# Kernel tuning notes

Measured on AMD Instinct MI355X. Metric: run time of the kernel, lower is better.

Reference implementation:

```python
import jax, jax.numpy as jnp
import numpy as np

BS, N1, N2, D = 2, 512, 512, 64  # in_dim = out_dim = D
TEMP = 1.0
EPS = 1e-5
POOL_RATIO = 0.5


def setup_inputs() -> dict:
    key = jax.random.key(0)
    ks = iter(jax.random.split(key, 32))
    nrm = lambda shape, s=0.05: jax.random.normal(next(ks), shape, dtype=jnp.float32) * s
    inp = {
        "x1": jax.random.normal(next(ks), (BS, N1, D), dtype=jnp.float32),
        "x2": jax.random.normal(next(ks), (BS, N2, D), dtype=jnp.float32),
        # proj_type1 / proj_type2 (Linear in->in); weights stored [in, out]
        "W1": nrm((D, D)), "b1": jnp.zeros((D,), jnp.float32),
        "W2": nrm((D, D)), "b2": jnp.zeros((D,), jnp.float32),
        # att_proj / att_projM (Linear in->out)
        "Wa": nrm((D, D)), "ba": jnp.zeros((D,), jnp.float32),
        "WaM": nrm((D, D)), "baM": jnp.zeros((D,), jnp.float32),
        # attention weight vectors (out_dim, 1)
        "w11": nrm((D, 1), 0.2), "w22": nrm((D, 1), 0.2),
        "w12": nrm((D, 1), 0.2), "wM": nrm((D, 1), 0.2),
        # projections
        "Wpa": nrm((D, D)), "bpa": jnp.zeros((D,), jnp.float32),
        "Wwoa": nrm((D, D)), "bwoa": jnp.zeros((D,), jnp.float32),
        "WpaM": nrm((D, D)), "bpaM": jnp.zeros((D,), jnp.float32),
        "WwoaM": nrm((D, D)), "bwoaM": jnp.zeros((D,), jnp.float32),
        # BatchNorm1d affine params
        "gamma": jnp.ones((D,), jnp.float32), "beta": jnp.zeros((D,), jnp.float32),
        # GraphPool score layer (Linear D->1), shared pool as in Model
        "Wp": nrm((D, 1), 0.2), "bp": jnp.zeros((1,), jnp.float32),
    }
    return inp


def _htrg_gat(x1, x2, W1, b1, W2, b2, Wa, ba, WaM, baM, w11, w22, w12, wM,
              Wpa, bpa, Wwoa, bwoa, WpaM, bpaM, WwoaM, bwoaM, gamma, beta):
    n1 = x1.shape[1]
    x1p = x1 @ W1 + b1
    x2p = x2 @ W2 + b2
    x = jnp.concatenate([x1p, x2p], axis=1)          # (b, N, d)
    master = jnp.mean(x, axis=1, keepdims=True)       # (b, 1, d)

    # --- attention map: pairwise node products, blockwise score weights ---
    pair = x[:, :, None, :] * x[:, None, :, :]        # (b, N, N, d)
    t = jnp.tanh(pair @ Wa + ba)                      # (b, N, N, d)
    top = jnp.concatenate([t[:, :n1, :n1] @ w11, t[:, :n1, n1:] @ w12], axis=2)
    bot = jnp.concatenate([t[:, n1:, :n1] @ w12, t[:, n1:, n1:] @ w22], axis=2)
    board = jnp.concatenate([top, bot], axis=1) / TEMP  # (b, N, N, 1)
    att = jax.nn.softmax(board, axis=-2)

    # --- master update ---
    tm = jnp.tanh((x * master) @ WaM + baM)           # (b, N, d)
    am = jax.nn.softmax((tm @ wM) / TEMP, axis=-2)    # (b, N, 1)
    agg_m = jnp.einsum('bn,bnd->bd', am[..., 0], x)[:, None, :]  # (b, 1, d)
    master_new = (agg_m @ WpaM + bpaM) + (master @ WwoaM + bwoaM)

    # --- project nodes with attention ---
    agg = jnp.einsum('bij,bjd->bid', att[..., 0], x)  # (b, N, d)
    xo = (agg @ Wpa + bpa) + (x @ Wwoa + bwoa)

    # --- BatchNorm1d over flattened (b*N) rows, then SELU ---
    mu = jnp.mean(xo, axis=(0, 1))
    var = jnp.var(xo, axis=(0, 1))
    xo = (xo - mu) * jax.lax.rsqrt(var + EPS) * gamma + beta
    xo = jax.nn.selu(xo)
    return xo[:, :n1], xo[:, n1:], master_new


def _graph_pool(x, Wp, bp):
    # scores -> sigmoid -> scale features -> top-k gather
    n = x.shape[1]
    k = max(int(n * POOL_RATIO), 1)
    scores = jax.nn.sigmoid(x @ Wp + bp)              # (b, n, 1)
    _, idx = jax.lax.top_k(scores[..., 0], k)         # (b, k)
    xs = x * scores
    return jnp.take_along_axis(xs, idx[..., None], axis=1)  # (b, k, d)


def reference(x1, x2, W1, b1, W2, b2, Wa, ba, WaM, baM, w11, w22, w12, wM,
              Wpa, bpa, Wwoa, bwoa, WpaM, bpaM, WwoaM, bwoaM, gamma, beta, Wp, bp):
    o1, o2, master = _htrg_gat(x1, x2, W1, b1, W2, b2, Wa, ba, WaM, baM,
                               w11, w22, w12, wM, Wpa, bpa, Wwoa, bwoa,
                               WpaM, bpaM, WwoaM, bwoaM, gamma, beta)
    p1 = _graph_pool(o1, Wp, bp)
    p2 = _graph_pool(o2, Wp, bp)
    return jnp.concatenate([p1, p2], axis=1)          # (b, n1/2 + n2/2, d)
```

## Files before the change

### kernel.cpp

```cpp
#include <hip/hip_runtime.h>

typedef float f32x4 __attribute__((ext_vector_type(4)));
typedef short short8 __attribute__((ext_vector_type(8)));
typedef short s16x4 __attribute__((ext_vector_type(4)));

#define N_TOT 1024
#define N_HALF 512
#define D 64
#define KPOOL 256

#if __has_builtin(__builtin_amdgcn_exp2f)
#define EXP2F(x) __builtin_amdgcn_exp2f(x)
#else
#define EXP2F(x) __expf((x) * 0.6931471805599453f)
#endif
#if __has_builtin(__builtin_amdgcn_rcpf)
#define RCPF(x) __builtin_amdgcn_rcpf(x)
#else
#define RCPF(x) (1.0f / (x))
#endif

__device__ __forceinline__ short f2bf(float v) {
    unsigned u = __float_as_uint(v);
    u += 0x7FFFu + ((u >> 16) & 1u);
    return (short)(u >> 16);
}
__device__ __forceinline__ float bf2f(unsigned short u) {
    return __uint_as_float(((unsigned)u) << 16);
}

__global__ void __launch_bounds__(64)
k_proj(const float* __restrict__ x1, const float* __restrict__ x2,
       const float* __restrict__ W1, const float* __restrict__ b1,
       const float* __restrict__ W2, const float* __restrict__ b2,
       float* __restrict__ x_f, unsigned short* __restrict__ x_bf,
       unsigned short* __restrict__ xT_hi, unsigned short* __restrict__ xT_lo) {
    int blk = blockIdx.x;
    int b = blk >> 8;
    int n0 = (blk & 255) * 4;
    int t = threadIdx.x;

    const float *src, *W, *bias;
    if (n0 < N_HALF) { src = x1 + (b * N_HALF + n0) * D;            W = W1; bias = b1; }
    else             { src = x2 + (b * N_HALF + (n0 - N_HALF)) * D; W = W2; bias = b2; }

    __shared__ float rows[4][D];
#pragma unroll
    for (int r = 0; r < 4; ++r) rows[r][t] = src[r * D + t];
    __syncthreads();

    float bv = bias[t];
    float acc[4];
#pragma unroll
    for (int r = 0; r < 4; ++r) acc[r] = bv;
    for (int d = 0; d < D; ++d) {
        float w = W[d * D + t];
#pragma unroll
        for (int r = 0; r < 4; ++r) acc[r] = fmaf(rows[r][d], w, acc[r]);
    }

    s16x4 hiv, lov;
#pragma unroll
    for (int r = 0; r < 4; ++r) {
        unsigned short hi = (unsigned short)f2bf(acc[r]);
        unsigned short lo = (unsigned short)f2bf(acc[r] - bf2f(hi));
        x_f[((size_t)b * N_TOT + n0 + r) * D + t] = acc[r];
        x_bf[((size_t)b * N_TOT + n0 + r) * D + t] = hi;
        hiv[r] = (short)hi; lov[r] = (short)lo;
    }
    *reinterpret_cast<s16x4*>(xT_hi + ((size_t)b * D + t) * N_TOT + n0) = hiv;
    *reinterpret_cast<s16x4*>(xT_lo + ((size_t)b * D + t) * N_TOT + n0) = lov;
}

__global__ void __launch_bounds__(256)
k_score(const float* __restrict__ x_f, const unsigned short* __restrict__ x_bf,
        const float* __restrict__ Wa, const float* __restrict__ ba,
        const float* __restrict__ w11, const float* __restrict__ w22,
        const float* __restrict__ w12, unsigned* __restrict__ Ep) {
    int bid = blockIdx.x;
    int b = bid >> 9, c = bid & 511;
    int tid = threadIdx.x;
    int l = tid & 63, wv = tid >> 6;
    int kc = l & 15, dg = l >> 4;

    const float C2 = 2.885390081777927f;
    const float LOG2E = 1.4426950408889634f;

    __shared__ float xi_s[D];
    const unsigned short* xb_b = x_bf + b * N_TOT * D;
    unsigned* Eb = Ep + ((size_t)b << 20);

#pragma unroll
    for (int phase = 0; phase < 2; ++phase) {
        int i = phase ? (N_TOT - 1 - c) : c;

        __syncthreads();
        if (tid < D) xi_s[tid] = x_f[(b * N_TOT + i) * D + tid];
        __syncthreads();

        const float* wTop = (i < N_HALF) ? w11 : w12;
        const float* wBot = (i < N_HALF) ? w12 : w22;

        short8 bfrag[4][2];
        float bac[4], wm2A[4], wm2B[4];
        float wsumA = 0.f, wsumB = 0.f;
#pragma unroll
        for (int kt = 0; kt < 4; ++kt) {
            int kcol = kt * 16 + kc;
            bac[kt] = ba[kcol] * C2;
            float wA = wTop[kcol], wB = wBot[kcol];
            wm2A[kt] = -2.f * wA; wm2B[kt] = -2.f * wB;
            wsumA += wA; wsumB += wB;
#pragma unroll
            for (int mm = 0; mm < 2; ++mm) {
                short8 f;
#pragma unroll
                for (int e = 0; e < 8; ++e) {
                    int d = mm * 32 + dg * 8 + e;
                    f[e] = f2bf(xi_s[d] * Wa[d * D + kcol]);
                }
                bfrag[kt][mm] = f;
            }
        }

        int jt0 = i >> 4;
        for (int jt = jt0 + wv; jt < 64; jt += 4) {
            const unsigned short* arow = xb_b + (jt * 16 + kc) * D + dg * 8;
            short8 a0 = *reinterpret_cast<const short8*>(arow);
            short8 a1 = *reinterpret_cast<const short8*>(arow + 32);
            f32x4 acc[4];
#pragma unroll
            for (int kt = 0; kt < 4; ++kt) {
                f32x4 z = {0.f, 0.f, 0.f, 0.f};
                z = __builtin_amdgcn_mfma_f32_16x16x32_bf16(a0, bfrag[kt][0], z, 0, 0, 0);
                z = __builtin_amdgcn_mfma_f32_16x16x32_bf16(a1, bfrag[kt][1], z, 0, 0, 0);
                acc[kt] = z;
            }
            bool top = (jt < 32);
            float wsum_t = top ? wsumA : wsumB;
#pragma unroll
            for (int r = 0; r < 4; ++r) {
                float part = wsum_t;
#pragma unroll
                for (int kt = 0; kt < 4; ++kt) {
                    float e2 = EXP2F(fmaf(acc[kt][r], C2, bac[kt]));
                    float rcv = RCPF(e2 + 1.f);
                    part = fmaf(top ? wm2A[kt] : wm2B[kt], rcv, part);
                }
                part += __shfl_xor(part, 1);
                part += __shfl_xor(part, 2);
                part += __shfl_xor(part, 4);
                part += __shfl_xor(part, 8);
                if (kc == 0) {
                    int j = jt * 16 + dg * 4 + r;
                    if (j >= i) {
                        float e = EXP2F(part * LOG2E);
                        unsigned short eh = (unsigned short)f2bf(e);
                        unsigned short el = (unsigned short)f2bf(e - bf2f(eh));
                        unsigned pk = ((unsigned)eh << 16) | (unsigned)el;
                        Eb[(size_t)i * N_TOT + j] = pk;
                        if (j > i) Eb[(size_t)j * N_TOT + i] = pk;
                    }
                }
            }
        }
    }
}

__global__ void __launch_bounds__(256)
k_aggp(const unsigned* __restrict__ Ep,
       const unsigned short* __restrict__ xT_hi, const unsigned short* __restrict__ xT_lo,
       float* __restrict__ pagg, float* __restrict__ rowsum_part) {
    int blk = blockIdx.x;
    int b = blk >> 7, rest = blk & 127;
    int it = rest >> 1, jh = rest & 1;
    int i0 = it * 16, jbase = jh * 512;
    int tid = threadIdx.x;
    int l = tid & 63, wv = tid >> 6;
    int kc = l & 15, dg = l >> 4;

    const unsigned* Eb = Ep + ((size_t)b << 20);
    const unsigned short* xTH = xT_hi + (size_t)b * D * N_TOT;
    const unsigned short* xTL = xT_lo + (size_t)b * D * N_TOT;

    f32x4 C0 = {0.f, 0.f, 0.f, 0.f}, C1 = C0, C2v = C0;
    const unsigned* Ap = Eb + (size_t)(i0 + kc) * N_TOT + jbase + dg * 8;
    const unsigned short* BH = xTH + (size_t)(wv * 16 + kc) * N_TOT + jbase + dg * 8;
    const unsigned short* BL = xTL + (size_t)(wv * 16 + kc) * N_TOT + jbase + dg * 8;
#pragma unroll 4
    for (int ks = 0; ks < 16; ++ks) {
        uint4 p0 = *reinterpret_cast<const uint4*>(Ap + ks * 32);
        uint4 p1 = *reinterpret_cast<const uint4*>(Ap + ks * 32 + 4);
        short8 ah, al;
        ah[0] = (short)(p0.x >> 16); al[0] = (short)(p0.x & 0xffff);
        ah[1] = (short)(p0.y >> 16); al[1] = (short)(p0.y & 0xffff);
        ah[2] = (short)(p0.z >> 16); al[2] = (short)(p0.z & 0xffff);
        ah[3] = (short)(p0.w >> 16); al[3] = (short)(p0.w & 0xffff);
        ah[4] = (short)(p1.x >> 16); al[4] = (short)(p1.x & 0xffff);
        ah[5] = (short)(p1.y >> 16); al[5] = (short)(p1.y & 0xffff);
        ah[6] = (short)(p1.z >> 16); al[6] = (short)(p1.z & 0xffff);
        ah[7] = (short)(p1.w >> 16); al[7] = (short)(p1.w & 0xffff);
        short8 bh = *reinterpret_cast<const short8*>(BH + ks * 32);
        short8 bl = *reinterpret_cast<const short8*>(BL + ks * 32);
        C0 = __builtin_amdgcn_mfma_f32_16x16x32_bf16(ah, bh, C0, 0, 0, 0);
        C1 = __builtin_amdgcn_mfma_f32_16x16x32_bf16(ah, bl, C1, 0, 0, 0);
        C2v = __builtin_amdgcn_mfma_f32_16x16x32_bf16(al, bh, C2v, 0, 0, 0);
    }
    f32x4 C = (C0 + C1) + C2v;

    {
        int row = wv * 4 + (l & 3);
        int seg = l >> 2;
        const unsigned* Er = Eb + (size_t)(i0 + row) * N_TOT + jbase + seg * 32;
        float rs = 0.f;
#pragma unroll
        for (int u = 0; u < 8; ++u) {
            uint4 v = *reinterpret_cast<const uint4*>(Er + u * 4);
            rs += __uint_as_float(v.x & 0xffff0000u) + __uint_as_float(v.x << 16);
            rs += __uint_as_float(v.y & 0xffff0000u) + __uint_as_float(v.y << 16);
            rs += __uint_as_float(v.z & 0xffff0000u) + __uint_as_float(v.z << 16);
            rs += __uint_as_float(v.w & 0xffff0000u) + __uint_as_float(v.w << 16);
        }
        rs += __shfl_xor(rs, 4);
        rs += __shfl_xor(rs, 8);
        rs += __shfl_xor(rs, 16);
        rs += __shfl_xor(rs, 32);
        if (l < 4) rowsum_part[(size_t)(b * 2 + jh) * N_TOT + i0 + wv * 4 + l] = rs;
    }

#pragma unroll
    for (int r = 0; r < 4; ++r)
        pagg[((size_t)(b * 2 + jh) * N_TOT + i0 + dg * 4 + r) * D + wv * 16 + kc] = C[r];
}

__global__ void __launch_bounds__(256)
k_aggfin(const float* __restrict__ pagg, const float* __restrict__ rowsum_part,
         const float* __restrict__ x_f,
         const float* __restrict__ Wpa, const float* __restrict__ bpa,
         const float* __restrict__ Wwoa, const float* __restrict__ bwoa,
         float* __restrict__ xo_pre, float* __restrict__ partials) {
    int b = blockIdx.x >> 6, it = blockIdx.x & 63;
    int i0 = it * 16;
    int tid = threadIdx.x;
    int l = tid & 63, wv = tid >> 6;

    __shared__ float aggL[16][D];
    __shared__ float xiL[16][D];
    __shared__ float xoL[16][D];
    __shared__ float riL[16];

    const float* p0 = pagg + ((size_t)(b * 2 + 0) * N_TOT + i0) * D;
    const float* p1 = pagg + ((size_t)(b * 2 + 1) * N_TOT + i0) * D;
    const float* xB = x_f + ((size_t)b * N_TOT + i0) * D;
#pragma unroll
    for (int u = 0; u < 4; ++u) {
        int idx = tid + u * 256;
        reinterpret_cast<float*>(aggL)[idx] = p0[idx] + p1[idx];
        reinterpret_cast<float*>(xiL)[idx] = xB[idx];
    }
    if (tid < 16)
        riL[tid] = 1.f / (rowsum_part[(size_t)(b * 2 + 0) * N_TOT + i0 + tid] +
                          rowsum_part[(size_t)(b * 2 + 1) * N_TOT + i0 + tid]);
    __syncthreads();
#pragma unroll
    for (int u = 0; u < 4; ++u) {
        int idx = tid + u * 256;
        reinterpret_cast<float*>(aggL)[idx] *= riL[idx >> 6];
    }
    __syncthreads();

    int k = l;
    float xo[4];
#pragma unroll
    for (int r = 0; r < 4; ++r) xo[r] = bpa[k] + bwoa[k];
    for (int dd = 0; dd < D; ++dd) {
        float wp = Wpa[dd * D + k], ww = Wwoa[dd * D + k];
#pragma unroll
        for (int r = 0; r < 4; ++r) {
            int row = wv * 4 + r;
            xo[r] += aggL[row][dd] * wp + xiL[row][dd] * ww;
        }
    }
#pragma unroll
    for (int r = 0; r < 4; ++r) {
        int row = wv * 4 + r;
        xo_pre[((size_t)b * N_TOT + i0 + row) * D + k] = xo[r];
        xoL[row][k] = xo[r];
    }
    __syncthreads();
    if (tid < D) {
        float s = 0.f, qv = 0.f;
#pragma unroll
        for (int mm = 0; mm < 16; ++mm) { float v = xoL[mm][tid]; s += v; qv = fmaf(v, v, qv); }
        partials[blockIdx.x * 128 + tid] = s;
        partials[blockIdx.x * 128 + 64 + tid] = qv;
    }
}

__global__ void k_stats2(const float* __restrict__ partials, float* __restrict__ stats) {
    int t = threadIdx.x;
    int g = t >> 7;
    int f128 = t & 127;
    float s = 0.f;
    for (int blk = g * 32; blk < g * 32 + 32; ++blk) s += partials[blk * 128 + f128];
    __shared__ float SQ[4][128];
    SQ[g][f128] = s;
    __syncthreads();
    if (t < 128) {
        float tot = SQ[0][t] + SQ[1][t] + SQ[2][t] + SQ[3][t];
        SQ[0][t] = tot;
    }
    __syncthreads();
    if (t < D) {
        float mu = SQ[0][t] * (1.f / 2048.f);
        float ex2 = SQ[0][64 + t] * (1.f / 2048.f);
        stats[t] = mu;
        stats[D + t] = rsqrtf(ex2 - mu * mu + 1e-5f);
    }
}

__global__ void k_norm(const float* __restrict__ xo_pre, const float* __restrict__ stats,
                       const float* __restrict__ gamma, const float* __restrict__ beta,
                       const float* __restrict__ Wp, const float* __restrict__ bp,
                       float* __restrict__ o_norm, float* __restrict__ scores) {
    int r = blockIdx.x * 4 + (threadIdx.x >> 6);
    int t = threadIdx.x & 63;
    float v = xo_pre[r * D + t];
    v = (v - stats[t]) * stats[D + t] * gamma[t] + beta[t];
    const float kScale = 1.0507009873554805f, kAlpha = 1.6732632423543772f;
    v = (v > 0.f) ? kScale * v : kScale * kAlpha * expm1f(v);
    o_norm[r * D + t] = v;
    float pd = v * Wp[t];
#pragma unroll
    for (int off = 32; off >= 1; off >>= 1) pd += __shfl_xor(pd, off);
    if (t == 0) scores[r] = 1.f / (1.f + __expf(-(pd + bp[0])));
}

__global__ void __launch_bounds__(512)
k_pool(const float* __restrict__ o_norm, const float* __restrict__ scores,
       float* __restrict__ out) {
    int b = blockIdx.x >> 1, half = blockIdx.x & 1;
    int tid = threadIdx.x;
    __shared__ float sc_s[N_HALF];
    __shared__ unsigned long long keys[N_HALF];
    __shared__ unsigned short map[KPOOL];

    {
        float sc = scores[b * N_TOT + half * N_HALF + tid];
        sc_s[tid] = sc;
        keys[tid] = ((unsigned long long)__float_as_uint(sc) << 10) | (unsigned)(511 - tid);
    }
    __syncthreads();
    unsigned long long mine = keys[tid];
    int cnt = 0;
#pragma unroll 8
    for (int qq = 0; qq < N_HALF; ++qq) cnt += (keys[qq] > mine) ? 1 : 0;
    if (cnt < KPOOL) map[cnt] = (unsigned short)tid;
    __syncthreads();
    int d = tid & 63;
    for (int rr = tid >> 6; rr < KPOOL; rr += 8) {
        int src = map[rr];
        out[(size_t)(b * N_HALF + half * KPOOL + rr) * D + d] =
            o_norm[(size_t)(b * N_TOT + half * N_HALF + src) * D + d] * sc_s[src];
    }
}

extern "C" void kernel_launch(void* const* d_in, const int* in_sizes, int n_in,
                              void* d_out, int out_size, void* d_ws, size_t ws_size,
                              hipStream_t stream) {
    const float* x1   = (const float*)d_in[0];
    const float* x2   = (const float*)d_in[1];
    const float* W1   = (const float*)d_in[2];
    const float* b1   = (const float*)d_in[3];
    const float* W2   = (const float*)d_in[4];
    const float* b2   = (const float*)d_in[5];
    const float* Wa   = (const float*)d_in[6];
    const float* ba   = (const float*)d_in[7];
    const float* w11  = (const float*)d_in[10];
    const float* w22  = (const float*)d_in[11];
    const float* w12  = (const float*)d_in[12];
    const float* Wpa  = (const float*)d_in[14];
    const float* bpa  = (const float*)d_in[15];
    const float* Wwoa = (const float*)d_in[16];
    const float* bwoa = (const float*)d_in[17];
    const float* gamma= (const float*)d_in[22];
    const float* beta = (const float*)d_in[23];
    const float* Wp   = (const float*)d_in[24];
    const float* bp   = (const float*)d_in[25];
    float* out = (float*)d_out;

    char* ws = (char*)d_ws;
    float*          x_f     = (float*)(ws + 0);
    unsigned short* x_bf    = (unsigned short*)(ws + 524288);
    unsigned short* xT_hi   = (unsigned short*)(ws + 786432);
    unsigned short* xT_lo   = (unsigned short*)(ws + 1048576);
    unsigned*       Ep      = (unsigned*)(ws + 1310720);
    float*          pagg    = (float*)(ws + 9699328);
    float*          rowsum  = (float*)(ws + 10747904);
    float*          xo_pre  = (float*)(ws + 10764288);
    float*          o_norm  = (float*)(ws + 11288576);
    float*          scores  = (float*)(ws + 11812864);
    float*          partials= (float*)(ws + 11821056);
    float*          stats   = (float*)(ws + 11886592);

    hipLaunchKernelGGL(k_proj, dim3(512), dim3(64), 0, stream,
                       x1, x2, W1, b1, W2, b2, x_f, x_bf, xT_hi, xT_lo);
    hipLaunchKernelGGL(k_score, dim3(1024), dim3(256), 0, stream,
                       x_f, x_bf, Wa, ba, w11, w22, w12, Ep);
    hipLaunchKernelGGL(k_aggp, dim3(256), dim3(256), 0, stream,
                       Ep, xT_hi, xT_lo, pagg, rowsum);
    hipLaunchKernelGGL(k_aggfin, dim3(128), dim3(256), 0, stream,
                       pagg, rowsum, x_f, Wpa, bpa, Wwoa, bwoa, xo_pre, partials);
    hipLaunchKernelGGL(k_stats2, dim3(1), dim3(512), 0, stream, partials, stats);
    hipLaunchKernelGGL(k_norm, dim3(512), dim3(256), 0, stream,
                       xo_pre, stats, gamma, beta, Wp, bp, o_norm, scores);
    hipLaunchKernelGGL(k_pool, dim3(4), dim3(512), 0, stream, o_norm, scores, out);
}
```

Measured before the change: 98.46 us.

## Split score rows into separate blocks and fuse stats, norm and pool kernels

The score kernel now launches one block per row i instead of pairing row c with row N-1-c inside a block. Rows are interleaved in reversed 256-row chunks so triangular work stays balanced, and the bias and tanh scale are folded into the MFMA accumulator init and the B fragments, which removes a per-element FMA. The BatchNorm stats, normalization/SELU/scoring and top-k pooling kernels are merged into a single 4-block tail kernel that recomputes the normalization only for the gathered rows. This cuts two launches and the o_norm and scores round-trips, but puts the whole tail on just 4 blocks and folds C2 into the bf16 weights, which slightly changes rounding.

```diff
diff --git a/kernel.cpp b/kernel.cpp
--- a/kernel.cpp
+++ b/kernel.cpp
@@ -78,89 +78,89 @@
         const float* __restrict__ w11, const float* __restrict__ w22,
         const float* __restrict__ w12, unsigned* __restrict__ Ep) {
     int bid = blockIdx.x;
-    int b = bid >> 9, c = bid & 511;
+    int b = bid >> 10, n = bid & 1023;
+    int q = n >> 8, c = n & 255;
+    int i = (q << 8) | ((q & 1) ? (255 - c) : c);
     int tid = threadIdx.x;
     int l = tid & 63, wv = tid >> 6;
     int kc = l & 15, dg = l >> 4;
 
+    __shared__ float xi_s[D];
+    if (tid < D) xi_s[tid] = x_f[(b * N_TOT + i) * D + tid];
+    __syncthreads();
+
     const float C2 = 2.885390081777927f;
     const float LOG2E = 1.4426950408889634f;
 
-    __shared__ float xi_s[D];
+    const float* wTop = (i < N_HALF) ? w11 : w12;
+    const float* wBot = (i < N_HALF) ? w12 : w22;
+
+    short8 bfrag[4][2];
+    f32x4 accinit[4];
+    float wm2A[4], wm2B[4];
+    float wsumA = 0.f, wsumB = 0.f;
+#pragma unroll
+    for (int kt = 0; kt < 4; ++kt) {
+        int kcol = kt * 16 + kc;
+        float bac = ba[kcol] * C2;
+        accinit[kt] = {bac, bac, bac, bac};
+        float wA = wTop[kcol], wB = wBot[kcol];
+        wm2A[kt] = -2.f * wA; wm2B[kt] = -2.f * wB;
+        wsumA += wA; wsumB += wB;
+#pragma unroll
+        for (int mm = 0; mm < 2; ++mm) {
+            short8 f;
+#pragma unroll
+            for (int e = 0; e < 8; ++e) {
+                int d = mm * 32 + dg * 8 + e;
+                f[e] = f2bf(xi_s[d] * Wa[d * D + kcol] * C2);
+            }
+            bfrag[kt][mm] = f;
+        }
+    }
+
     const unsigned short* xb_b = x_bf + b * N_TOT * D;
     unsigned* Eb = Ep + ((size_t)b << 20);
-
-#pragma unroll
-    for (int phase = 0; phase < 2; ++phase) {
-        int i = phase ? (N_TOT - 1 - c) : c;
-
-        __syncthreads();
-        if (tid < D) xi_s[tid] = x_f[(b * N_TOT + i) * D + tid];
-        __syncthreads();
-
-        const float* wTop = (i < N_HALF) ? w11 : w12;
-        const float* wBot = (i < N_HALF) ? w12 : w22;
-
-        short8 bfrag[4][2];
-        float bac[4], wm2A[4], wm2B[4];
-        float wsumA = 0.f, wsumB = 0.f;
+    int jt0 = i >> 4;
+    for (int jt = jt0 + wv; jt < 64; jt += 4) {
+        const unsigned short* arow = xb_b + (jt * 16 + kc) * D + dg * 8;
+        short8 a0 = *reinterpret_cast<const short8*>(arow);
+        short8 a1 = *reinterpret_cast<const short8*>(arow + 32);
+        f32x4 acc[4];
 #pragma unroll
         for (int kt = 0; kt < 4; ++kt) {
-            int kcol = kt * 16 + kc;
-            bac[kt] = ba[kcol] * C2;
-            float wA = wTop[kcol], wB = wBot[kcol];
-            wm2A[kt] = -2.f * wA; wm2B[kt] = -2.f * wB;
-            wsumA += wA; wsumB += wB;
-#pragma unroll
-            for (int mm = 0; mm < 2; ++mm) {
-                short8 f;
-#pragma unroll
-                for (int e = 0; e < 8; ++e) {
-                    int d = mm * 32 + dg * 8 + e;
-                    f[e] = f2bf(xi_s[d] * Wa[d * D + kcol]);
-                }
-                bfrag[kt][mm] = f;
+            f32x4 z = accinit[kt];
+            z = __builtin_amdgcn_mfma_f32_16x16x32_bf16(a0, bfrag[kt][0], z, 0, 0, 0);
+            z = __builtin_amdgcn_mfma_f32_16x16x32_bf16(a1, bfrag[kt][1], z, 0, 0, 0);
+            acc[kt] = z;
+        }
+        bool top = (jt < 32);
+        float wsum_t = top ? wsumA : wsumB;
+        float wm2s[4];
+#pragma unroll
+        for (int kt = 0; kt < 4; ++kt) wm2s[kt] = top ? wm2A[kt] : wm2B[kt];
+#pragma unroll
+        for (int r = 0; r < 4; ++r) {
+            float part = wsum_t;
+#pragma unroll
+            for (int kt = 0; kt < 4; ++kt) {
+                float e2 = EXP2F(acc[kt][r]);
+                float rcv = RCPF(e2 + 1.f);
+                part = fmaf(wm2s[kt], rcv, part);
             }
-        }
-
-        int jt0 = i >> 4;
-        for (int jt = jt0 + wv; jt < 64; jt += 4) {
-            const unsigned short* arow = xb_b + (jt * 16 + kc) * D + dg * 8;
-            short8 a0 = *reinterpret_cast<const short8*>(arow);
-            short8 a1 = *reinterpret_cast<const short8*>(arow + 32);
-            f32x4 acc[4];
-#pragma unroll
-            for (int kt = 0; kt < 4; ++kt) {
-                f32x4 z = {0.f, 0.f, 0.f, 0.f};
-                z = __builtin_amdgcn_mfma_f32_16x16x32_bf16(a0, bfrag[kt][0], z, 0, 0, 0);
-                z = __builtin_amdgcn_mfma_f32_16x16x32_bf16(a1, bfrag[kt][1], z, 0, 0, 0);
-                acc[kt] = z;
-            }
-            bool top = (jt < 32);
-            float wsum_t = top ? wsumA : wsumB;
-#pragma unroll
-            for (int r = 0; r < 4; ++r) {
-                float part = wsum_t;
-#pragma unroll
-                for (int kt = 0; kt < 4; ++kt) {
-                    float e2 = EXP2F(fmaf(acc[kt][r], C2, bac[kt]));
-                    float rcv = RCPF(e2 + 1.f);
-                    part = fmaf(top ? wm2A[kt] : wm2B[kt], rcv, part);
-                }
-                part += __shfl_xor(part, 1);
-                part += __shfl_xor(part, 2);
-                part += __shfl_xor(part, 4);
-                part += __shfl_xor(part, 8);
-                if (kc == 0) {
-                    int j = jt * 16 + dg * 4 + r;
-                    if (j >= i) {
-                        float e = EXP2F(part * LOG2E);
-                        unsigned short eh = (unsigned short)f2bf(e);
-                        unsigned short el = (unsigned short)f2bf(e - bf2f(eh));
-                        unsigned pk = ((unsigned)eh << 16) | (unsigned)el;
-                        Eb[(size_t)i * N_TOT + j] = pk;
-                        if (j > i) Eb[(size_t)j * N_TOT + i] = pk;
-                    }
+            part += __shfl_xor(part, 1);
+            part += __shfl_xor(part, 2);
+            part += __shfl_xor(part, 4);
+            part += __shfl_xor(part, 8);
+            if (kc == 0) {
+                int j = jt * 16 + dg * 4 + r;
+                if (j >= i) {
+                    float e = EXP2F(part * LOG2E);
+                    unsigned short eh = (unsigned short)f2bf(e);
+                    unsigned short el = (unsigned short)f2bf(e - bf2f(eh));
+                    unsigned pk = ((unsigned)eh << 16) | (unsigned)el;
+                    Eb[(size_t)i * N_TOT + j] = pk;
+                    if (j > i) Eb[(size_t)j * N_TOT + i] = pk;
                 }
             }
         }
@@ -297,71 +297,81 @@
     }
 }
 
-__global__ void k_stats2(const float* __restrict__ partials, float* __restrict__ stats) {
-    int t = threadIdx.x;
-    int g = t >> 7;
-    int f128 = t & 127;
-    float s = 0.f;
-    for (int blk = g * 32; blk < g * 32 + 32; ++blk) s += partials[blk * 128 + f128];
-    __shared__ float SQ[4][128];
-    SQ[g][f128] = s;
-    __syncthreads();
-    if (t < 128) {
-        float tot = SQ[0][t] + SQ[1][t] + SQ[2][t] + SQ[3][t];
-        SQ[0][t] = tot;
-    }
-    __syncthreads();
-    if (t < D) {
-        float mu = SQ[0][t] * (1.f / 2048.f);
-        float ex2 = SQ[0][64 + t] * (1.f / 2048.f);
-        stats[t] = mu;
-        stats[D + t] = rsqrtf(ex2 - mu * mu + 1e-5f);
-    }
-}
-
-__global__ void k_norm(const float* __restrict__ xo_pre, const float* __restrict__ stats,
-                       const float* __restrict__ gamma, const float* __restrict__ beta,
-                       const float* __restrict__ Wp, const float* __restrict__ bp,
-                       float* __restrict__ o_norm, float* __restrict__ scores) {
-    int r = blockIdx.x * 4 + (threadIdx.x >> 6);
-    int t = threadIdx.x & 63;
-    float v = xo_pre[r * D + t];
-    v = (v - stats[t]) * stats[D + t] * gamma[t] + beta[t];
-    const float kScale = 1.0507009873554805f, kAlpha = 1.6732632423543772f;
-    v = (v > 0.f) ? kScale * v : kScale * kAlpha * expm1f(v);
-    o_norm[r * D + t] = v;
-    float pd = v * Wp[t];
-#pragma unroll
-    for (int off = 32; off >= 1; off >>= 1) pd += __shfl_xor(pd, off);
-    if (t == 0) scores[r] = 1.f / (1.f + __expf(-(pd + bp[0])));
-}
-
-__global__ void __launch_bounds__(512)
-k_pool(const float* __restrict__ o_norm, const float* __restrict__ scores,
+__global__ void __launch_bounds__(1024)
+k_tail(const float* __restrict__ xo_pre, const float* __restrict__ partials,
+       const float* __restrict__ gamma, const float* __restrict__ beta,
+       const float* __restrict__ Wp, const float* __restrict__ bp,
        float* __restrict__ out) {
     int b = blockIdx.x >> 1, half = blockIdx.x & 1;
-    int tid = threadIdx.x;
+    int t = threadIdx.x;
+    int d = t & 63;
+    int wvg = t >> 6;
+
+    __shared__ float SQ[8][128];
+    __shared__ float muL[D], rsL[D];
     __shared__ float sc_s[N_HALF];
     __shared__ unsigned long long keys[N_HALF];
     __shared__ unsigned short map[KPOOL];
 
     {
-        float sc = scores[b * N_TOT + half * N_HALF + tid];
-        sc_s[tid] = sc;
-        keys[tid] = ((unsigned long long)__float_as_uint(sc) << 10) | (unsigned)(511 - tid);
-    }
-    __syncthreads();
-    unsigned long long mine = keys[tid];
-    int cnt = 0;
+        int g = t >> 7, f = t & 127;
+        float s = 0.f;
+        for (int blk = g; blk < 128; blk += 8) s += partials[blk * 128 + f];
+        SQ[g][f] = s;
+        __syncthreads();
+        if (t < 128) {
+            float tot = 0.f;
+#pragma unroll
+            for (int g2 = 0; g2 < 8; ++g2) tot += SQ[g2][t];
+            SQ[0][t] = tot;
+        }
+        __syncthreads();
+        if (t < D) {
+            float mu = SQ[0][t] * (1.f / 2048.f);
+            float ex2 = SQ[0][64 + t] * (1.f / 2048.f);
+            muL[t] = mu;
+            rsL[t] = rsqrtf(ex2 - mu * mu + 1e-5f);
+        }
+        __syncthreads();
+    }
+
+    const float kScale = 1.0507009873554805f, kAlpha = 1.6732632423543772f;
+    int base = b * N_TOT + half * N_HALF;
+    float mu = muL[d], rs = rsL[d], gm = gamma[d], bt = beta[d], wp = Wp[d];
+    float bpv = bp[0];
+
+    for (int u = 0; u < 32; ++u) {
+        int r = wvg * 32 + u;
+        float v = xo_pre[(size_t)(base + r) * D + d];
+        v = (v - mu) * rs * gm + bt;
+        v = (v > 0.f) ? kScale * v : kScale * kAlpha * expm1f(v);
+        float pd = v * wp;
+#pragma unroll
+        for (int off = 32; off >= 1; off >>= 1) pd += __shfl_xor(pd, off);
+        if (d == 0) {
+            float sc = 1.f / (1.f + __expf(-(pd + bpv)));
+            sc_s[r] = sc;
+            keys[r] = ((unsigned long long)__float_as_uint(sc) << 10) | (unsigned)(511 - r);
+        }
+    }
+    __syncthreads();
+
+    if (t < N_HALF) {
+        unsigned long long mine = keys[t];
+        int cnt = 0;
 #pragma unroll 8
-    for (int qq = 0; qq < N_HALF; ++qq) cnt += (keys[qq] > mine) ? 1 : 0;
-    if (cnt < KPOOL) map[cnt] = (unsigned short)tid;
-    __syncthreads();
-    int d = tid & 63;
-    for (int rr = tid >> 6; rr < KPOOL; rr += 8) {
+        for (int qq = 0; qq < N_HALF; ++qq) cnt += (keys[qq] > mine) ? 1 : 0;
+        if (cnt < KPOOL) map[cnt] = (unsigned short)t;
+    }
+    __syncthreads();
+
+    for (int u = 0; u < 16; ++u) {
+        int rr = wvg + u * 16;
         int src = map[rr];
-        out[(size_t)(b * N_HALF + half * KPOOL + rr) * D + d] =
-            o_norm[(size_t)(b * N_TOT + half * N_HALF + src) * D + d] * sc_s[src];
+        float v = xo_pre[(size_t)(base + src) * D + d];
+        v = (v - mu) * rs * gm + bt;
+        v = (v > 0.f) ? kScale * v : kScale * kAlpha * expm1f(v);
+        out[(size_t)(b * N_HALF + half * KPOOL + rr) * D + d] = v * sc_s[src];
     }
 }
 
@@ -398,21 +408,16 @@
     float*          pagg    = (float*)(ws + 9699328);
     float*          rowsum  = (float*)(ws + 10747904);
     float*          xo_pre  = (float*)(ws + 10764288);
-    float*          o_norm  = (float*)(ws + 11288576);
-    float*          scores  = (float*)(ws + 11812864);
-    float*          partials= (float*)(ws + 11821056);
-    float*          stats   = (float*)(ws + 11886592);
+    float*          partials= (float*)(ws + 11288576);
 
     hipLaunchKernelGGL(k_proj, dim3(512), dim3(64), 0, stream,
                        x1, x2, W1, b1, W2, b2, x_f, x_bf, xT_hi, xT_lo);
-    hipLaunchKernelGGL(k_score, dim3(1024), dim3(256), 0, stream,
+    hipLaunchKernelGGL(k_score, dim3(2048), dim3(256), 0, stream,
                        x_f, x_bf, Wa, ba, w11, w22, w12, Ep);
     hipLaunchKernelGGL(k_aggp, dim3(256), dim3(256), 0, stream,
                        Ep, xT_hi, xT_lo, pagg, rowsum);
     hipLaunchKernelGGL(k_aggfin, dim3(128), dim3(256), 0, stream,
                        pagg, rowsum, x_f, Wpa, bpa, Wwoa, bwoa, xo_pre, partials);
-    hipLaunchKernelGGL(k_stats2, dim3(1), dim3(512), 0, stream, partials, stats);
-    hipLaunchKernelGGL(k_norm, dim3(512), dim3(256), 0, stream,
-                       xo_pre, stats, gamma, beta, Wp, bp, o_norm, scores);
-    hipLaunchKernelGGL(k_pool, dim3(4), dim3(512), 0, stream, o_norm, scores, out);
-}
+    hipLaunchKernelGGL(k_tail, dim3(4), dim3(1024), 0, stream,
+                       xo_pre, partials, gamma, beta, Wp, bp, out);
+}
```

Result: slower. 107.1 us (+8.8%).
